# Kernel optimization log

Hardware: AMD Instinct MI355X
Metric: run time of the kernel (lower is better)

Reference implementation:

```python
import jax, jax.numpy as jnp
import numpy as np

MB, T, NP1, D, K = 512, 256, 201, 4, 5
CTX = D + 4  # context_dim = amp_dim + 4


def setup_inputs() -> dict:
    key = jax.random.key(0)
    ks = jax.random.split(key, 10)
    demands = jax.random.uniform(ks[0], (MB, NP1)) * 9.0 + 1.0
    demands = demands.at[:, 0].set(0.0)  # depot has zero demand
    coords = jax.random.uniform(ks[1], (MB, NP1, 2))
    psi_prime = jax.random.normal(ks[2], (MB, NP1, D))
    knn_indices = jax.random.randint(ks[3], (MB, NP1, K), 0, NP1)
    actions = jax.random.randint(ks[4], (MB, T), 0, NP1)
    Wq_w = jax.random.normal(ks[5], (D, CTX)) * 0.1
    Wq_b = jax.random.normal(ks[6], (D,)) * 0.1
    return {
        'demands': demands, 'coords': coords, 'psi_prime': psi_prime,
        'Wq_w': Wq_w, 'Wq_b': Wq_b,
        'lambda_param': jnp.float32(0.1), 'mu_param': jnp.float32(0.5),
        'nu_param': jnp.float32(0.1),
        'actions': actions, 'knn_indices': knn_indices, 'capacity': 50,
    }


def _forward(demands, coords, psi_prime, Wq_w, Wq_b,
             lambda_param, mu_param, nu_param,
             actions, knn_indices, capacity):
    mb, T = actions.shape
    np1 = psi_prime.shape[1]
    n_customers = np1 - 1
    cap = max(float(capacity), 1e-8)
    b_idx = jnp.arange(mb)

    # --- sequential state bookkeeping (cur node, used capacity, visited mask) ---
    def step(carry, act_t):
        cur, used, vis = carry
        out = (cur, used, vis)  # state BEFORE applying action t
        at_depot = act_t == 0
        dem_t = demands[b_idx, act_t]
        used_n = jnp.where(at_depot, 0.0, used + dem_t)
        vis_n = vis.at[b_idx, act_t].set(True).at[:, 0].set(False)
        return (act_t, used_n, vis_n), out

    init = (jnp.zeros(mb, jnp.int32), jnp.zeros(mb, demands.dtype),
            jnp.zeros((mb, np1), bool))
    _, (all_cur, all_used, all_vis) = jax.lax.scan(step, init,
                                                   actions.T.astype(jnp.int32))
    all_cur = all_cur.T                       # [mb,T]
    all_used = all_used.T                     # [mb,T]
    all_vis = jnp.transpose(all_vis, (1, 0, 2))  # [mb,T,np1]

    remaining = cap - all_used
    cap_norm = remaining / cap
    exceeds = demands[:, None, :] > remaining[:, :, None]   # [mb,T,np1]
    mask = (all_vis | exceeds).at[:, :, 0].set(False)
    at_depot3 = all_cur == 0
    has_cust = (~mask[:, :, 1:]).any(-1)
    mask = mask.at[:, :, 0].set(at_depot3 & has_cust)

    cur_coords = coords[b_idx[:, None], all_cur]            # [mb,T,2]
    psi_curr = psi_prime[b_idx[:, None], all_cur]           # [mb,T,D]
    psi_curr = jnp.where(at_depot3[..., None], 0.0, psi_curr)
    t_norm = jnp.broadcast_to(
        (jnp.arange(T, dtype=psi_prime.dtype) / max(n_customers, 1))[None, :],
        (mb, T))
    ctx = jnp.concatenate([psi_curr, cap_norm[..., None],
                           t_norm[..., None], cur_coords], -1)  # [mb,T,D+4]
    query = ctx @ Wq_w.T + Wq_b                              # [mb,T,D]
    context_scores = jnp.einsum('btd,bnd->btn', query, psi_prime)

    # kNN interference: psi is fixed over t, so compute once and broadcast
    neigh = psi_prime[b_idx[:, None, None], knn_indices]     # [mb,np1,K,D]
    interference = jnp.einsum('bnd,bnkd->bn', psi_prime, neigh)  # [mb,np1]

    diff = coords[:, None, :, :] - cur_coords[:, :, None, :]  # [mb,T,np1,2]
    dist = jnp.sqrt(jnp.sum(diff * diff, -1) + 1e-12)         # [mb,T,np1]

    mu = jnp.clip(mu_param, 0.0, 20.0)
    lam = jnp.clip(lambda_param, -2.0, 3.0)
    nu = jnp.clip(nu_param, -2.0, 3.0)
    scores = (context_scores + lam * interference[:, None, :]
              - mu * dist + nu * (demands[:, None, :] / cap))
    scores = jnp.where(mask, -1e9, scores)
    lp3 = jax.nn.log_softmax(scores, -1)                      # [mb,T,np1]
    lp_new = jnp.take_along_axis(lp3, actions[:, :, None], 2)[..., 0]
    entropy = (-(jnp.exp(lp3) * lp3).sum(-1)).mean(1)         # [mb]
    return lp_new, entropy


def reference(demands, coords, psi_prime, Wq_w, Wq_b,
              lambda_param, mu_param, nu_param,
              actions, knn_indices, capacity):
    return _forward(demands, coords, psi_prime, Wq_w, Wq_b,
                    lambda_param, mu_param, nu_param,
                    actions, knn_indices, capacity)
```

## Files before the change

kernel.cpp:

```cpp
#include <hip/hip_runtime.h>
#include <hip/hip_bf16.h>
#include <math.h>

#define MB 512
#define T 256
#define NP1 201
#define KNN 5

typedef unsigned long long u64;
typedef unsigned int u32;

__global__ __launch_bounds__(256, 8) void fused_kernel(
        const float* __restrict__ demands,
        const float* __restrict__ coords,
        const float* __restrict__ psi,
        const float* __restrict__ Wq_w,
        const float* __restrict__ Wq_b,
        const float* __restrict__ lam_p,
        const float* __restrict__ mu_p,
        const float* __restrict__ nu_p,
        const int* __restrict__ actions,
        const int* __restrict__ knn,
        const int* __restrict__ cap_p,
        float* __restrict__ lp_out,
        float* __restrict__ ent_out) {
    __shared__ float4 psiL[NP1];
    __shared__ float4 zCL[NP1];
    __shared__ u64   visW[4][T];
    __shared__ float remL[T];
    __shared__ int   actL[T];
    __shared__ float demL[T];
    __shared__ u64   aggV[4][4];
    __shared__ int   aggD[4];
    __shared__ float entPart[4];

    const int blk = blockIdx.x;
    const int b = blk >> 2, chunk = blk & 3;
    const int tid = threadIdx.x;
    const int lane = tid & 63, wv = tid >> 6;

    const float cap = fmaxf((float)cap_p[0], 1e-8f);

    const int t = tid;
    const int a_t = actions[b * T + t];
    actL[t] = a_t;
    demL[t] = demands[b * NP1 + a_t];

    u64 m0 = (a_t < 64)                ? (1ull << a_t)         : 0ull;
    u64 m1 = (a_t >= 64 && a_t < 128)  ? (1ull << (a_t - 64))  : 0ull;
    u64 m2 = (a_t >= 128 && a_t < 192) ? (1ull << (a_t - 128)) : 0ull;
    u64 m3 = (a_t >= 192)              ? (1ull << (a_t - 192)) : 0ull;
    int d = (a_t == 0) ? t : -1;

    float4 packP, packC;
    if (t < NP1) {
        const float lam = fminf(fmaxf(lam_p[0], -2.f), 3.f);
        const float nu  = fminf(fmaxf(nu_p[0],  -2.f), 3.f);
        const float4 pn = *(const float4*)(psi + ((size_t)b * NP1 + t) * 4);
        const float2 cc2 = *(const float2*)(coords + ((size_t)b * NP1 + t) * 2);
        float interf = 0.f;
        const int* kn = knn + ((size_t)b * NP1 + t) * KNN;
#pragma unroll
        for (int k = 0; k < KNN; ++k) {
            const int j = kn[k];
            const float4 pj = *(const float4*)(psi + ((size_t)b * NP1 + j) * 4);
            interf += pn.x * pj.x + pn.y * pj.y + pn.z * pj.z + pn.w * pj.w;
        }
        const float dem = demands[b * NP1 + t];
        packP = pn;
        packC.x = lam * interf + nu * (dem / cap);
        packC.y = cc2.x; packC.z = cc2.y; packC.w = dem;
    }

#pragma unroll
    for (int off = 1; off < 64; off <<= 1) {
        m0 |= __shfl_up(m0, off);
        m1 |= __shfl_up(m1, off);
        m2 |= __shfl_up(m2, off);
        m3 |= __shfl_up(m3, off);
        d = max(d, __shfl_up(d, off));
    }
    if (lane == 63) {
        aggV[0][wv] = m0; aggV[1][wv] = m1;
        aggV[2][wv] = m2; aggV[3][wv] = m3;
        aggD[wv] = d;
    }
    __syncthreads();

    u64 p0 = 0, p1 = 0, p2 = 0, p3 = 0; int pd = -1;
    for (int u = 0; u < wv; ++u) {
        p0 |= aggV[0][u]; p1 |= aggV[1][u];
        p2 |= aggV[2][u]; p3 |= aggV[3][u];
        pd = max(pd, aggD[u]);
    }
    m0 |= p0; m1 |= p1; m2 |= p2; m3 |= p3; d = max(d, pd);
    visW[0][t] = m0; visW[1][t] = m1; visW[2][t] = m2; visW[3][t] = m3;

    int dPrev = __shfl_up(d, 1);
    if (lane == 0) dPrev = pd;
    const int s = dPrev + 1;

    float used = 0.f;
    for (int j = s; j < t; ++j) used += demL[j];
    remL[t] = cap - used;

    if (t < NP1) { psiL[t] = packP; zCL[t] = packC; }
    __syncthreads();

    const int rloc = tid >> 2, split = tid & 3;
    const int tr = chunk * 64 + rloc;

    const float rem = remL[tr];
    const int a_row = actL[tr];
    const int cur = (tr == 0) ? 0 : actL[tr - 1];
    const bool at_depot = (cur == 0);
    u64 v0 = 0, v1 = 0, v2 = 0, v3 = 0;
    if (tr > 0) {
        v0 = visW[0][tr - 1] & ~1ull;
        v1 = visW[1][tr - 1];
        v2 = visW[2][tr - 1];
        v3 = visW[3][tr - 1];
    }

    const float mu  = fminf(fmaxf(mu_p[0], 0.f), 20.f);
    const float capn = rem / cap;
    const float tn = (float)tr / 200.f;

    float4 pc = psiL[cur];
    if (at_depot) { pc.x = 0.f; pc.y = 0.f; pc.z = 0.f; pc.w = 0.f; }
    const float4 cz = zCL[cur];
    const float ccx = cz.y, ccy = cz.z;

    float q0, q1, q2, q3;
    {
        const float c0 = pc.x, c1 = pc.y, c2 = pc.z, c3 = pc.w;
        q0 = Wq_b[0] + Wq_w[0]*c0 + Wq_w[1]*c1 + Wq_w[2]*c2 + Wq_w[3]*c3
           + Wq_w[4]*capn + Wq_w[5]*tn + Wq_w[6]*ccx + Wq_w[7]*ccy;
        q1 = Wq_b[1] + Wq_w[8]*c0 + Wq_w[9]*c1 + Wq_w[10]*c2 + Wq_w[11]*c3
           + Wq_w[12]*capn + Wq_w[13]*tn + Wq_w[14]*ccx + Wq_w[15]*ccy;
        q2 = Wq_b[2] + Wq_w[16]*c0 + Wq_w[17]*c1 + Wq_w[18]*c2 + Wq_w[19]*c3
           + Wq_w[20]*capn + Wq_w[21]*tn + Wq_w[22]*ccx + Wq_w[23]*ccy;
        q3 = Wq_b[3] + Wq_w[24]*c0 + Wq_w[25]*c1 + Wq_w[26]*c2 + Wq_w[27]*c3
           + Wq_w[28]*capn + Wq_w[29]*tn + Wq_w[30]*ccx + Wq_w[31]*ccy;
    }

    const int base = 1 + split * 50;
    const int wsel = base >> 6;
    const u64 wlo = (wsel == 0) ? v0 : (wsel == 1) ? v1 : v2;
    const u64 whi = (wsel == 0) ? v1 : (wsel == 1) ? v2 : v3;
    const int off = base & 63;
    u64 window = (wlo >> off) | (whi << (64 - off));

    float S = 0.f, W = 0.f;
#pragma unroll 10
    for (int i = 0; i < 50; ++i) {
        const int n = base + i;
        const float4 p4 = psiL[n];
        const float4 c4 = zCL[n];
        float sco = fmaf(q0, p4.x, fmaf(q1, p4.y, fmaf(q2, p4.z, fmaf(q3, p4.w, c4.x))));
        const float dx = c4.y - ccx, dy = c4.z - ccy;
        sco = fmaf(-mu, __builtin_amdgcn_sqrtf(fmaf(dx, dx, fmaf(dy, dy, 1e-12f))), sco);
        const bool maskn = (((u32)(window >> i)) & 1u) || (c4.w > rem);
        const float e = maskn ? 0.f : __expf(sco);
        S += e;
        W = fmaf(e, sco, W);
    }

    S += __shfl_xor(S, 1); S += __shfl_xor(S, 2);
    W += __shfl_xor(W, 1); W += __shfl_xor(W, 2);

    const bool hasCust = S > 0.f;

    float entv = 0.f;
    if (split == 0) {
        {
            const float4 p4 = psiL[0];
            const float4 c4 = zCL[0];
            float sco = fmaf(q0, p4.x, fmaf(q1, p4.y, fmaf(q2, p4.z, fmaf(q3, p4.w, c4.x))));
            const float dx = c4.y - ccx, dy = c4.z - ccy;
            sco = fmaf(-mu, __builtin_amdgcn_sqrtf(fmaf(dx, dx, fmaf(dy, dy, 1e-12f))), sco);
            const bool mk = at_depot && hasCust;
            const float e = mk ? 0.f : __expf(sco);
            S += e;
            W = fmaf(e, sco, W);
        }
        const float L = __logf(S);
        const float4 p4 = psiL[a_row];
        const float4 c4 = zCL[a_row];
        float sco = fmaf(q0, p4.x, fmaf(q1, p4.y, fmaf(q2, p4.z, fmaf(q3, p4.w, c4.x))));
        const float dx = c4.y - ccx, dy = c4.z - ccy;
        sco = fmaf(-mu, __builtin_amdgcn_sqrtf(fmaf(dx, dx, fmaf(dy, dy, 1e-12f))), sco);
        bool maskA;
        if (a_row == 0) {
            maskA = at_depot && hasCust;
        } else {
            const u64 vw = (a_row < 64) ? v0 : (a_row < 128) ? v1
                         : (a_row < 192) ? v2 : v3;
            maskA = ((vw >> (a_row & 63)) & 1ull) || (c4.w > rem);
        }
        const float sAct = maskA ? -1e9f : sco;
        lp_out[b * T + tr] = sAct - L;
        entv = L - W / S;
    }

#pragma unroll
    for (int o = 32; o > 0; o >>= 1) entv += __shfl_xor(entv, o);
    if (lane == 0) entPart[wv] = entv;
    __syncthreads();
    if (tid == 0) {
        const float tot = entPart[0] + entPart[1] + entPart[2] + entPart[3];
        atomicAdd(ent_out + b, tot * (1.f / (float)T));
    }
}

__global__ __launch_bounds__(512) void zero_ent_kernel(float* __restrict__ ent_out) {
    const int b = threadIdx.x;
    if (b < MB) ent_out[b] = 0.f;
}

extern "C" void kernel_launch(void* const* d_in, const int* in_sizes, int n_in,
                              void* d_out, int out_size, void* d_ws, size_t ws_size,
                              hipStream_t stream) {
    const float* demands = (const float*)d_in[0];
    const float* coords  = (const float*)d_in[1];
    const float* psi     = (const float*)d_in[2];
    const float* Wq_w    = (const float*)d_in[3];
    const float* Wq_b    = (const float*)d_in[4];
    const float* lam_p   = (const float*)d_in[5];
    const float* mu_p    = (const float*)d_in[6];
    const float* nu_p    = (const float*)d_in[7];
    const int*   actions = (const int*)d_in[8];
    const int*   knn     = (const int*)d_in[9];
    const int*   cap_p   = (const int*)d_in[10];

    float* lp_out  = (float*)d_out;
    float* ent_out = lp_out + MB * T;

    (void)d_ws; (void)ws_size;

    zero_ent_kernel<<<1, 512, 0, stream>>>(ent_out);
    fused_kernel<<<MB * 4, 256, 0, stream>>>(
        demands, coords, psi, Wq_w, Wq_b, lam_p, mu_p, nu_p,
        actions, knn, cap_p, lp_out, ent_out);
}
```

Before: 109.6 us.

## Process all four time-chunks per block to avoid redundant setup work

Each block now handles one batch element and all 256 time rows, so every thread computes four rows, instead of four blocks per batch each rerunning the scan, prefix and KNN setup. The per-node psi and context loads from LDS are reused across the four rows inside the inner loop. Because each block now owns its whole batch entry, entropy is written directly, which removes the atomicAdd and the separate zeroing kernel launch. In exchange there are 512 blocks instead of 2048, register pressure per thread is higher, and launch bounds are relaxed to two blocks per CU.

```diff
diff --git a/kernel.cpp b/kernel.cpp
--- a/kernel.cpp
+++ b/kernel.cpp
@@ -10,7 +10,7 @@
 typedef unsigned long long u64;
 typedef unsigned int u32;
 
-__global__ __launch_bounds__(256, 8) void fused_kernel(
+__global__ __launch_bounds__(256, 2) void fused_kernel(
         const float* __restrict__ demands,
         const float* __restrict__ coords,
         const float* __restrict__ psi,
@@ -34,8 +34,7 @@
     __shared__ int   aggD[4];
     __shared__ float entPart[4];
 
-    const int blk = blockIdx.x;
-    const int b = blk >> 2, chunk = blk & 3;
+    const int b = blockIdx.x;
     const int tid = threadIdx.x;
     const int lane = tid & 63, wv = tid >> 6;
 
@@ -108,114 +107,121 @@
     __syncthreads();
 
     const int rloc = tid >> 2, split = tid & 3;
-    const int tr = chunk * 64 + rloc;
-
-    const float rem = remL[tr];
-    const int a_row = actL[tr];
-    const int cur = (tr == 0) ? 0 : actL[tr - 1];
-    const bool at_depot = (cur == 0);
-    u64 v0 = 0, v1 = 0, v2 = 0, v3 = 0;
-    if (tr > 0) {
-        v0 = visW[0][tr - 1] & ~1ull;
-        v1 = visW[1][tr - 1];
-        v2 = visW[2][tr - 1];
-        v3 = visW[3][tr - 1];
-    }
-
     const float mu  = fminf(fmaxf(mu_p[0], 0.f), 20.f);
-    const float capn = rem / cap;
-    const float tn = (float)tr / 200.f;
-
-    float4 pc = psiL[cur];
-    if (at_depot) { pc.x = 0.f; pc.y = 0.f; pc.z = 0.f; pc.w = 0.f; }
-    const float4 cz = zCL[cur];
-    const float ccx = cz.y, ccy = cz.z;
-
-    float q0, q1, q2, q3;
-    {
-        const float c0 = pc.x, c1 = pc.y, c2 = pc.z, c3 = pc.w;
-        q0 = Wq_b[0] + Wq_w[0]*c0 + Wq_w[1]*c1 + Wq_w[2]*c2 + Wq_w[3]*c3
-           + Wq_w[4]*capn + Wq_w[5]*tn + Wq_w[6]*ccx + Wq_w[7]*ccy;
-        q1 = Wq_b[1] + Wq_w[8]*c0 + Wq_w[9]*c1 + Wq_w[10]*c2 + Wq_w[11]*c3
-           + Wq_w[12]*capn + Wq_w[13]*tn + Wq_w[14]*ccx + Wq_w[15]*ccy;
-        q2 = Wq_b[2] + Wq_w[16]*c0 + Wq_w[17]*c1 + Wq_w[18]*c2 + Wq_w[19]*c3
-           + Wq_w[20]*capn + Wq_w[21]*tn + Wq_w[22]*ccx + Wq_w[23]*ccy;
-        q3 = Wq_b[3] + Wq_w[24]*c0 + Wq_w[25]*c1 + Wq_w[26]*c2 + Wq_w[27]*c3
-           + Wq_w[28]*capn + Wq_w[29]*tn + Wq_w[30]*ccx + Wq_w[31]*ccy;
-    }
 
     const int base = 1 + split * 50;
     const int wsel = base >> 6;
-    const u64 wlo = (wsel == 0) ? v0 : (wsel == 1) ? v1 : v2;
-    const u64 whi = (wsel == 0) ? v1 : (wsel == 1) ? v2 : v3;
-    const int off = base & 63;
-    u64 window = (wlo >> off) | (whi << (64 - off));
-
-    float S = 0.f, W = 0.f;
-#pragma unroll 10
+    const int woff = base & 63;
+
+    float q0[4], q1[4], q2[4], q3[4], ccx[4], ccy[4], remA[4];
+    u64 window[4];
+    bool adep[4];
+#pragma unroll
+    for (int c = 0; c < 4; ++c) {
+        const int tr = c * 64 + rloc;
+        const float rem = remL[tr];
+        remA[c] = rem;
+        const int cur = (tr == 0) ? 0 : actL[tr - 1];
+        const bool at_depot = (cur == 0);
+        adep[c] = at_depot;
+
+        u64 wlo = 0, whi = 0;
+        if (tr > 0) {
+            wlo = visW[wsel][tr - 1];
+            whi = (wsel < 3) ? visW[wsel + 1][tr - 1] : 0ull;
+        }
+        window[c] = (wlo >> woff) | (whi << (64 - woff));
+
+        float4 pc = psiL[cur];
+        if (at_depot) { pc.x = 0.f; pc.y = 0.f; pc.z = 0.f; pc.w = 0.f; }
+        const float4 cz = zCL[cur];
+        ccx[c] = cz.y; ccy[c] = cz.z;
+
+        const float capn = rem / cap;
+        const float tn = (float)tr / 200.f;
+        const float c0 = pc.x, c1 = pc.y, c2 = pc.z, c3 = pc.w;
+        q0[c] = Wq_b[0] + Wq_w[0]*c0 + Wq_w[1]*c1 + Wq_w[2]*c2 + Wq_w[3]*c3
+              + Wq_w[4]*capn + Wq_w[5]*tn + Wq_w[6]*ccx[c] + Wq_w[7]*ccy[c];
+        q1[c] = Wq_b[1] + Wq_w[8]*c0 + Wq_w[9]*c1 + Wq_w[10]*c2 + Wq_w[11]*c3
+              + Wq_w[12]*capn + Wq_w[13]*tn + Wq_w[14]*ccx[c] + Wq_w[15]*ccy[c];
+        q2[c] = Wq_b[2] + Wq_w[16]*c0 + Wq_w[17]*c1 + Wq_w[18]*c2 + Wq_w[19]*c3
+              + Wq_w[20]*capn + Wq_w[21]*tn + Wq_w[22]*ccx[c] + Wq_w[23]*ccy[c];
+        q3[c] = Wq_b[3] + Wq_w[24]*c0 + Wq_w[25]*c1 + Wq_w[26]*c2 + Wq_w[27]*c3
+              + Wq_w[28]*capn + Wq_w[29]*tn + Wq_w[30]*ccx[c] + Wq_w[31]*ccy[c];
+    }
+
+    float S[4] = {0.f, 0.f, 0.f, 0.f};
+    float W[4] = {0.f, 0.f, 0.f, 0.f};
+#pragma unroll 5
     for (int i = 0; i < 50; ++i) {
         const int n = base + i;
         const float4 p4 = psiL[n];
         const float4 c4 = zCL[n];
-        float sco = fmaf(q0, p4.x, fmaf(q1, p4.y, fmaf(q2, p4.z, fmaf(q3, p4.w, c4.x))));
-        const float dx = c4.y - ccx, dy = c4.z - ccy;
-        sco = fmaf(-mu, __builtin_amdgcn_sqrtf(fmaf(dx, dx, fmaf(dy, dy, 1e-12f))), sco);
-        const bool maskn = (((u32)(window >> i)) & 1u) || (c4.w > rem);
-        const float e = maskn ? 0.f : __expf(sco);
-        S += e;
-        W = fmaf(e, sco, W);
-    }
-
-    S += __shfl_xor(S, 1); S += __shfl_xor(S, 2);
-    W += __shfl_xor(W, 1); W += __shfl_xor(W, 2);
-
-    const bool hasCust = S > 0.f;
+#pragma unroll
+        for (int c = 0; c < 4; ++c) {
+            float sco = fmaf(q0[c], p4.x, fmaf(q1[c], p4.y,
+                        fmaf(q2[c], p4.z, fmaf(q3[c], p4.w, c4.x))));
+            const float dx = c4.y - ccx[c], dy = c4.z - ccy[c];
+            sco = fmaf(-mu, __builtin_amdgcn_sqrtf(fmaf(dx, dx, fmaf(dy, dy, 1e-12f))), sco);
+            const bool maskn = (((u32)(window[c] >> i)) & 1u) || (c4.w > remA[c]);
+            const float e = maskn ? 0.f : __expf(sco);
+            S[c] += e;
+            W[c] = fmaf(e, sco, W[c]);
+        }
+    }
+
+#pragma unroll
+    for (int c = 0; c < 4; ++c) {
+        S[c] += __shfl_xor(S[c], 1); S[c] += __shfl_xor(S[c], 2);
+        W[c] += __shfl_xor(W[c], 1); W[c] += __shfl_xor(W[c], 2);
+    }
 
     float entv = 0.f;
     if (split == 0) {
-        {
-            const float4 p4 = psiL[0];
-            const float4 c4 = zCL[0];
-            float sco = fmaf(q0, p4.x, fmaf(q1, p4.y, fmaf(q2, p4.z, fmaf(q3, p4.w, c4.x))));
-            const float dx = c4.y - ccx, dy = c4.z - ccy;
+        const float4 pD = psiL[0];
+        const float4 zD = zCL[0];
+#pragma unroll
+        for (int c = 0; c < 4; ++c) {
+            const int tr = c * 64 + rloc;
+            const bool hasCust = S[c] > 0.f;
+            {
+                float sco = fmaf(q0[c], pD.x, fmaf(q1[c], pD.y,
+                            fmaf(q2[c], pD.z, fmaf(q3[c], pD.w, zD.x))));
+                const float dx = zD.y - ccx[c], dy = zD.z - ccy[c];
+                sco = fmaf(-mu, __builtin_amdgcn_sqrtf(fmaf(dx, dx, fmaf(dy, dy, 1e-12f))), sco);
+                const bool mk = adep[c] && hasCust;
+                const float e = mk ? 0.f : __expf(sco);
+                S[c] += e;
+                W[c] = fmaf(e, sco, W[c]);
+            }
+            const float L = __logf(S[c]);
+            const int a_row = actL[tr];
+            const float4 p4 = psiL[a_row];
+            const float4 c4 = zCL[a_row];
+            float sco = fmaf(q0[c], p4.x, fmaf(q1[c], p4.y,
+                        fmaf(q2[c], p4.z, fmaf(q3[c], p4.w, c4.x))));
+            const float dx = c4.y - ccx[c], dy = c4.z - ccy[c];
             sco = fmaf(-mu, __builtin_amdgcn_sqrtf(fmaf(dx, dx, fmaf(dy, dy, 1e-12f))), sco);
-            const bool mk = at_depot && hasCust;
-            const float e = mk ? 0.f : __expf(sco);
-            S += e;
-            W = fmaf(e, sco, W);
-        }
-        const float L = __logf(S);
-        const float4 p4 = psiL[a_row];
-        const float4 c4 = zCL[a_row];
-        float sco = fmaf(q0, p4.x, fmaf(q1, p4.y, fmaf(q2, p4.z, fmaf(q3, p4.w, c4.x))));
-        const float dx = c4.y - ccx, dy = c4.z - ccy;
-        sco = fmaf(-mu, __builtin_amdgcn_sqrtf(fmaf(dx, dx, fmaf(dy, dy, 1e-12f))), sco);
-        bool maskA;
-        if (a_row == 0) {
-            maskA = at_depot && hasCust;
-        } else {
-            const u64 vw = (a_row < 64) ? v0 : (a_row < 128) ? v1
-                         : (a_row < 192) ? v2 : v3;
-            maskA = ((vw >> (a_row & 63)) & 1ull) || (c4.w > rem);
-        }
-        const float sAct = maskA ? -1e9f : sco;
-        lp_out[b * T + tr] = sAct - L;
-        entv = L - W / S;
+            bool maskA;
+            if (a_row == 0) {
+                maskA = adep[c] && hasCust;
+            } else {
+                const u64 vw = (tr > 0) ? visW[a_row >> 6][tr - 1] : 0ull;
+                maskA = ((vw >> (a_row & 63)) & 1ull) || (c4.w > remA[c]);
+            }
+            const float sAct = maskA ? -1e9f : sco;
+            lp_out[b * T + tr] = sAct - L;
+            entv += L - W[c] / S[c];
+        }
     }
 
 #pragma unroll
     for (int o = 32; o > 0; o >>= 1) entv += __shfl_xor(entv, o);
     if (lane == 0) entPart[wv] = entv;
     __syncthreads();
-    if (tid == 0) {
-        const float tot = entPart[0] + entPart[1] + entPart[2] + entPart[3];
-        atomicAdd(ent_out + b, tot * (1.f / (float)T));
-    }
-}
-
-__global__ __launch_bounds__(512) void zero_ent_kernel(float* __restrict__ ent_out) {
-    const int b = threadIdx.x;
-    if (b < MB) ent_out[b] = 0.f;
+    if (tid == 0)
+        ent_out[b] = (entPart[0] + entPart[1] + entPart[2] + entPart[3])
+                     * (1.f / (float)T);
 }
 
 extern "C" void kernel_launch(void* const* d_in, const int* in_sizes, int n_in,
@@ -238,8 +244,7 @@
 
     (void)d_ws; (void)ws_size;
 
-    zero_ent_kernel<<<1, 512, 0, stream>>>(ent_out);
-    fused_kernel<<<MB * 4, 256, 0, stream>>>(
+    fused_kernel<<<MB, 256, 0, stream>>>(
         demands, coords, psi, Wq_w, Wq_b, lam_p, mu_p, nu_p,
         actions, knn, cap_p, lp_out, ent_out);
 }
```

Result: faster. 103.5 us (-5.5%).
